# Optimization experiments

Hardware: AMD Instinct MI355X
Metric: run time of the kernel (lower is better)

Reference implementation:

```python
import jax, jax.numpy as jnp
import numpy as np

GROUP_SIZE = 64

def setup_inputs() -> dict:
    key = jax.random.key(0)
    ks = jax.random.split(key, 7)
    T, N, K, NG = 4096, 4096, 11264, 4096 // GROUP_SIZE
    x = jax.random.normal(ks[0], (T, N), dtype=jnp.float32)
    Q = jax.random.randint(ks[1], (K, N), 0, 8, dtype=jnp.int32)  # uint8 3-bit codes
    scales = jax.random.uniform(ks[2], (K, NG), dtype=jnp.float32)
    zeros = jax.random.uniform(ks[3], (K, NG), dtype=jnp.float32) * 7.0
    mu1 = jax.random.uniform(ks[4], (N,), dtype=jnp.float32) + 0.5
    mu2 = jax.random.uniform(ks[5], (K,), dtype=jnp.float32) + 0.5
    bias = jax.random.normal(ks[6], (K,), dtype=jnp.float32)
    return {"x": x, "Q": Q, "scales": scales, "zeros": zeros, "mu1": mu1, "mu2": mu2, "bias": bias}

def reference(x, Q, scales, zeros, mu1, mu2, bias):
    K, N = Q.shape
    ng = scales.shape[1]
    # group-wise dequant: (Q - zero) * scale, groups along N
    Qg = Q.astype(jnp.float32).reshape(K, ng, GROUP_SIZE)
    W_deq_norm = ((Qg - zeros[:, :, None]) * scales[:, :, None]).reshape(K, N)
    # Sinkhorn mu rescale: per-row mu2, per-column mu1
    W_deq = W_deq_norm * mu2[:, None] * mu1[None, :]
    out = x @ W_deq.T + bias
    return out
```

## Files before the change

kernel.cpp:

```cpp
#include <hip/hip_runtime.h>
#include <stdint.h>
#include <stddef.h>


typedef __attribute__((ext_vector_type(8))) short bfrag;
typedef __attribute__((ext_vector_type(4))) float f32x4;
typedef __attribute__((ext_vector_type(4))) int   i32x4;

__device__ __forceinline__ short f2bf(float f) {
    uint32_t u = __float_as_uint(f);
    u += 0x7fffu + ((u >> 16) & 1u);
    return (short)(u >> 16);
}

__device__ __forceinline__ void gload_lds16(const void* g, void* l) {
    __builtin_amdgcn_global_load_lds(
        (const __attribute__((address_space(1))) void*)g,
        (__attribute__((address_space(3))) void*)l,
        16, 0, 0);
}

__global__ void cvt_x_kernel(const float* __restrict__ x, short* __restrict__ xb) {
    int i = blockIdx.x * 256 + threadIdx.x;
    const f32x4* xv = (const f32x4*)x;
    f32x4 a = xv[2 * i];
    f32x4 b = xv[2 * i + 1];
    bfrag o;
    o[0] = f2bf(a[0]); o[1] = f2bf(a[1]); o[2] = f2bf(a[2]); o[3] = f2bf(a[3]);
    o[4] = f2bf(b[0]); o[5] = f2bf(b[1]); o[6] = f2bf(b[2]); o[7] = f2bf(b[3]);
    ((bfrag*)xb)[i] = o;
}

__global__ void deq_w_kernel(const int* __restrict__ Q,
                             const float* __restrict__ scales,
                             const float* __restrict__ zeros,
                             const float* __restrict__ mu1,
                             const float* __restrict__ mu2,
                             short* __restrict__ wb,
                             int k0, int N, int NG) {
    int kl = blockIdx.y;
    int kg = k0 + kl;
    int c  = blockIdx.x * 256 + threadIdx.x;
    int n0 = c << 3;
    int g  = n0 >> 6;
    float s = scales[(size_t)kg * NG + g] * mu2[kg];
    float z = zeros[(size_t)kg * NG + g];
    const i32x4* qv = (const i32x4*)(Q + (size_t)kg * N + n0);
    i32x4 q0 = qv[0];
    i32x4 q1 = qv[1];
    const f32x4* uv = (const f32x4*)(mu1 + n0);
    f32x4 u0 = uv[0];
    f32x4 u1 = uv[1];
    bfrag o;
    o[0] = f2bf(((float)q0[0] - z) * s * u0[0]);
    o[1] = f2bf(((float)q0[1] - z) * s * u0[1]);
    o[2] = f2bf(((float)q0[2] - z) * s * u0[2]);
    o[3] = f2bf(((float)q0[3] - z) * s * u0[3]);
    o[4] = f2bf(((float)q1[0] - z) * s * u1[0]);
    o[5] = f2bf(((float)q1[1] - z) * s * u1[1]);
    o[6] = f2bf(((float)q1[2] - z) * s * u1[2]);
    o[7] = f2bf(((float)q1[3] - z) * s * u1[3]);
    ((bfrag*)wb)[(size_t)kl * (N >> 3) + c] = o;
}

#define BM 128
#define BN 128
#define BK 32

__global__ void gemm_bt_kernel(const short* __restrict__ A,
                               const short* __restrict__ B,
                               const float* __restrict__ bias,
                               float* __restrict__ C,
                               int Kc, int Nout, int col0) {
    __shared__ __attribute__((aligned(16))) short As[BM * BK];
    __shared__ __attribute__((aligned(16))) short Bs[BN * BK];

    const int tid  = threadIdx.x;
    const int lane = tid & 63;
    const int wave = tid >> 6;
    const int wm   = (wave >> 1) * 64;
    const int wn   = (wave & 1) * 64;
    const int bm   = blockIdx.y * BM;
    const int bnl  = blockIdx.x * BN;

    f32x4 acc[4][4];
#pragma unroll
    for (int i = 0; i < 4; i++)
#pragma unroll
        for (int j = 0; j < 4; j++)
            acc[i][j] = (f32x4){0.f, 0.f, 0.f, 0.f};

    const short* gA  = A + (size_t)(bm + (tid >> 2)) * Kc + (tid & 3) * 8;
    const short* gA2 = gA + (size_t)64 * Kc;
    const short* gB  = B + (size_t)(bnl + (tid >> 2)) * Kc + (tid & 3) * 8;
    const short* gB2 = gB + (size_t)64 * Kc;
    short* lA  = As + tid * 8;
    short* lA2 = As + 2048 + tid * 8;
    short* lB  = Bs + tid * 8;
    short* lB2 = Bs + 2048 + tid * 8;

    const int r  = lane & 15;
    const int ko = (lane >> 4) * 8;
    const short* pa = As + (wm + r) * BK + ko;
    const short* pb = Bs + (wn + r) * BK + ko;

    for (int k0 = 0; k0 < Kc; k0 += BK) {
        gload_lds16(gA + k0, lA);
        gload_lds16(gA2 + k0, lA2);
        gload_lds16(gB + k0, lB);
        gload_lds16(gB2 + k0, lB2);
        __syncthreads();

        bfrag af[4], bfv[4];
#pragma unroll
        for (int i = 0; i < 4; i++) af[i]  = *(const bfrag*)(pa + i * 16 * BK);
#pragma unroll
        for (int j = 0; j < 4; j++) bfv[j] = *(const bfrag*)(pb + j * 16 * BK);

#pragma unroll
        for (int i = 0; i < 4; i++)
#pragma unroll
            for (int j = 0; j < 4; j++)
                acc[i][j] = __builtin_amdgcn_mfma_f32_16x16x32_bf16(
                    af[i], bfv[j], acc[i][j], 0, 0, 0);

        __syncthreads();
    }

    const int row0  = bm + wm + (lane >> 4) * 4;
    const int colg0 = col0 + bnl + wn;
#pragma unroll
    for (int j = 0; j < 4; j++) {
        int col  = colg0 + j * 16 + r;
        float bv = bias[col];
#pragma unroll
        for (int i = 0; i < 4; i++) {
            int row = row0 + i * 16;
#pragma unroll
            for (int q = 0; q < 4; q++)
                C[(size_t)(row + q) * Nout + col] = acc[i][j][q] + bv;
        }
    }
}

__global__ void naive_kernel(const float* __restrict__ x, const int* __restrict__ Q,
                             const float* __restrict__ scales, const float* __restrict__ zeros,
                             const float* __restrict__ mu1, const float* __restrict__ mu2,
                             const float* __restrict__ bias, float* __restrict__ out,
                             int T, int N, int K, int NG) {
    long long total = (long long)T * K;
    for (long long idx = blockIdx.x * 256ll + threadIdx.x; idx < total;
         idx += (long long)gridDim.x * 256ll) {
        int t = (int)(idx / K);
        int k = (int)(idx - (long long)t * K);
        float s = 0.f;
        for (int n = 0; n < N; n++) {
            int g = n >> 6;
            float w = ((float)Q[(size_t)k * N + n] - zeros[(size_t)k * NG + g]) *
                      scales[(size_t)k * NG + g];
            s += x[(size_t)t * N + n] * w * mu1[n];
        }
        out[idx] = s * mu2[k] + bias[k];
    }
}

extern "C" void kernel_launch(void* const* d_in, const int* in_sizes, int n_in,
                              void* d_out, int out_size, void* d_ws, size_t ws_size,
                              hipStream_t stream) {
    const float* x      = (const float*)d_in[0];
    const int*   Q      = (const int*)d_in[1];
    const float* scales = (const float*)d_in[2];
    const float* zeros  = (const float*)d_in[3];
    const float* mu1    = (const float*)d_in[4];
    const float* mu2    = (const float*)d_in[5];
    const float* bias   = (const float*)d_in[6];
    float* out = (float*)d_out;

    const int N  = in_sizes[4];
    const int K  = in_sizes[5];
    const int T  = in_sizes[0] / N;
    const int NG = in_sizes[2] / K;

    const size_t xb_bytes  = (size_t)T * N * 2;
    const size_t row_bytes = (size_t)N * 2;

    if (ws_size < xb_bytes + 128 * row_bytes) {
        naive_kernel<<<4096, 256, 0, stream>>>(x, Q, scales, zeros, mu1, mu2,
                                               bias, out, T, N, K, NG);
        return;
    }

    short* xb = (short*)d_ws;
    short* wb = (short*)((char*)d_ws + xb_bytes);
    size_t max_rows = (ws_size - xb_bytes) / row_bytes;
    int CH = (int)((max_rows / 128) * 128);
    if (CH > K) CH = K;

    cvt_x_kernel<<<(T * N / 8) / 256, 256, 0, stream>>>(x, xb);

    for (int c0 = 0; c0 < K; c0 += CH) {
        int rows = (K - c0 < CH) ? (K - c0) : CH;
        dim3 dgrid(N / (8 * 256), rows);
        deq_w_kernel<<<dgrid, 256, 0, stream>>>(Q, scales, zeros, mu1, mu2, wb,
                                                c0, N, NG);
        dim3 ggrid(rows / BN, T / BM);
        gemm_bt_kernel<<<ggrid, 256, 0, stream>>>(xb, wb, bias, out, N, K, c0);
    }
}
```

Measured before the change: 791.4 us.

## Replace GEMM with 256x256 tile, double-buffered, swizzled-LDS 8-phase pipelined kernel

Replaces the 128x128x32 single-buffered GEMM with a 512-thread 256x256x64 kernel. It double-buffers 128KB of LDS, uses an XOR-swizzled LDS layout to avoid bank conflicts, and interleaves global-to-LDS loads with MFMA phases using s_setprio and fine-grained waitcnt. It also remaps blocks for L2 locality and widens the convert and dequant kernels to 16 elements per thread. The aim is to raise arithmetic intensity and overlap memory with compute, at the cost of high register and LDS use and a stricter shape requirement.

```diff
diff --git a/kernel.cpp b/kernel.cpp
--- a/kernel.cpp
+++ b/kernel.cpp
@@ -21,14 +21,16 @@
 }
 
 __global__ void cvt_x_kernel(const float* __restrict__ x, short* __restrict__ xb) {
-    int i = blockIdx.x * 256 + threadIdx.x;
-    const f32x4* xv = (const f32x4*)x;
-    f32x4 a = xv[2 * i];
-    f32x4 b = xv[2 * i + 1];
-    bfrag o;
-    o[0] = f2bf(a[0]); o[1] = f2bf(a[1]); o[2] = f2bf(a[2]); o[3] = f2bf(a[3]);
-    o[4] = f2bf(b[0]); o[5] = f2bf(b[1]); o[6] = f2bf(b[2]); o[7] = f2bf(b[3]);
-    ((bfrag*)xb)[i] = o;
+    size_t i = (size_t)blockIdx.x * 256 + threadIdx.x;
+    const f32x4* xv = (const f32x4*)x + 4 * i;
+    f32x4 a = xv[0], b = xv[1], c = xv[2], d = xv[3];
+    bfrag o0, o1;
+    o0[0] = f2bf(a[0]); o0[1] = f2bf(a[1]); o0[2] = f2bf(a[2]); o0[3] = f2bf(a[3]);
+    o0[4] = f2bf(b[0]); o0[5] = f2bf(b[1]); o0[6] = f2bf(b[2]); o0[7] = f2bf(b[3]);
+    o1[0] = f2bf(c[0]); o1[1] = f2bf(c[1]); o1[2] = f2bf(c[2]); o1[3] = f2bf(c[3]);
+    o1[4] = f2bf(d[0]); o1[5] = f2bf(d[1]); o1[6] = f2bf(d[2]); o1[7] = f2bf(d[3]);
+    bfrag* ov = (bfrag*)xb + 2 * i;
+    ov[0] = o0; ov[1] = o1;
 }
 
 __global__ void deq_w_kernel(const int* __restrict__ Q,
@@ -38,106 +40,149 @@
                              const float* __restrict__ mu2,
                              short* __restrict__ wb,
                              int k0, int N, int NG) {
-    int kl = blockIdx.y;
-    int kg = k0 + kl;
-    int c  = blockIdx.x * 256 + threadIdx.x;
-    int n0 = c << 3;
-    int g  = n0 >> 6;
-    float s = scales[(size_t)kg * NG + g] * mu2[kg];
-    float z = zeros[(size_t)kg * NG + g];
+    const int kl = blockIdx.x;
+    const int kg = k0 + kl;
+    const int t  = threadIdx.x;
+    const int n0 = t << 4;
+    const int g  = n0 >> 6;
+    const float s = scales[(size_t)kg * NG + g] * mu2[kg];
+    const float z = zeros[(size_t)kg * NG + g];
     const i32x4* qv = (const i32x4*)(Q + (size_t)kg * N + n0);
-    i32x4 q0 = qv[0];
-    i32x4 q1 = qv[1];
     const f32x4* uv = (const f32x4*)(mu1 + n0);
-    f32x4 u0 = uv[0];
-    f32x4 u1 = uv[1];
-    bfrag o;
-    o[0] = f2bf(((float)q0[0] - z) * s * u0[0]);
-    o[1] = f2bf(((float)q0[1] - z) * s * u0[1]);
-    o[2] = f2bf(((float)q0[2] - z) * s * u0[2]);
-    o[3] = f2bf(((float)q0[3] - z) * s * u0[3]);
-    o[4] = f2bf(((float)q1[0] - z) * s * u1[0]);
-    o[5] = f2bf(((float)q1[1] - z) * s * u1[1]);
-    o[6] = f2bf(((float)q1[2] - z) * s * u1[2]);
-    o[7] = f2bf(((float)q1[3] - z) * s * u1[3]);
-    ((bfrag*)wb)[(size_t)kl * (N >> 3) + c] = o;
-}
-
-#define BM 128
-#define BN 128
-#define BK 32
-
-__global__ void gemm_bt_kernel(const short* __restrict__ A,
-                               const short* __restrict__ B,
-                               const float* __restrict__ bias,
-                               float* __restrict__ C,
-                               int Kc, int Nout, int col0) {
-    __shared__ __attribute__((aligned(16))) short As[BM * BK];
-    __shared__ __attribute__((aligned(16))) short Bs[BN * BK];
+    i32x4 q0 = qv[0], q1 = qv[1], q2 = qv[2], q3 = qv[3];
+    f32x4 u0 = uv[0], u1 = uv[1], u2 = uv[2], u3 = uv[3];
+    bfrag o0, o1;
+    o0[0] = f2bf(((float)q0[0] - z) * s * u0[0]);
+    o0[1] = f2bf(((float)q0[1] - z) * s * u0[1]);
+    o0[2] = f2bf(((float)q0[2] - z) * s * u0[2]);
+    o0[3] = f2bf(((float)q0[3] - z) * s * u0[3]);
+    o0[4] = f2bf(((float)q1[0] - z) * s * u1[0]);
+    o0[5] = f2bf(((float)q1[1] - z) * s * u1[1]);
+    o0[6] = f2bf(((float)q1[2] - z) * s * u1[2]);
+    o0[7] = f2bf(((float)q1[3] - z) * s * u1[3]);
+    o1[0] = f2bf(((float)q2[0] - z) * s * u2[0]);
+    o1[1] = f2bf(((float)q2[1] - z) * s * u2[1]);
+    o1[2] = f2bf(((float)q2[2] - z) * s * u2[2]);
+    o1[3] = f2bf(((float)q2[3] - z) * s * u2[3]);
+    o1[4] = f2bf(((float)q3[0] - z) * s * u3[0]);
+    o1[5] = f2bf(((float)q3[1] - z) * s * u3[1]);
+    o1[6] = f2bf(((float)q3[2] - z) * s * u3[2]);
+    o1[7] = f2bf(((float)q3[3] - z) * s * u3[3]);
+    bfrag* ov = (bfrag*)(wb + (size_t)kl * N + n0);
+    ov[0] = o0; ov[1] = o1;
+}
+
+
+__global__ __launch_bounds__(512, 2)
+void gemm8p_kernel(const short* __restrict__ A, const short* __restrict__ B,
+                   const float* __restrict__ bias, float* __restrict__ C,
+                   int Kc, int Nout, int col0, int GX) {
+    extern __shared__ __attribute__((aligned(16))) char smem[];
 
     const int tid  = threadIdx.x;
     const int lane = tid & 63;
-    const int wave = tid >> 6;
-    const int wm   = (wave >> 1) * 64;
-    const int wn   = (wave & 1) * 64;
-    const int bm   = blockIdx.y * BM;
-    const int bnl  = blockIdx.x * BN;
-
-    f32x4 acc[4][4];
-#pragma unroll
-    for (int i = 0; i < 4; i++)
+    const int wid  = tid >> 6;
+    const int wm   = wid >> 2;
+    const int wn   = wid & 3;
+    const int r    = lane & 15;
+    const int hib  = (lane >> 4) << 4;
+    const int sw   = (r & 7) << 4;
+
+    const int nwg = (int)gridDim.x;
+    const int cpx = nwg >> 3;
+    const int bid = (int)blockIdx.x;
+    const int swz = (bid & 7) * cpx + (bid >> 3);
+    const int bx  = swz % GX;
+    const int by  = swz / GX;
+    const int bm  = by * 256;
+    const int bnl = bx * 256;
+
+    const int KB = Kc * 2;
+    const int swcol = ((tid ^ (tid >> 3)) & 7) << 4;
+    const char* srcA = (const char*)A + (size_t)(bm  + (tid >> 3)) * KB + swcol;
+    const char* srcB = (const char*)B + (size_t)(bnl + (tid >> 3)) * KB + swcol;
+
+    f32x4 acc[8][4];
+#pragma unroll
+    for (int i = 0; i < 8; i++)
 #pragma unroll
         for (int j = 0; j < 4; j++)
             acc[i][j] = (f32x4){0.f, 0.f, 0.f, 0.f};
 
-    const short* gA  = A + (size_t)(bm + (tid >> 2)) * Kc + (tid & 3) * 8;
-    const short* gA2 = gA + (size_t)64 * Kc;
-    const short* gB  = B + (size_t)(bnl + (tid >> 2)) * Kc + (tid & 3) * 8;
-    const short* gB2 = gB + (size_t)64 * Kc;
-    short* lA  = As + tid * 8;
-    short* lA2 = As + 2048 + tid * 8;
-    short* lB  = Bs + tid * 8;
-    short* lB2 = Bs + 2048 + tid * 8;
-
-    const int r  = lane & 15;
-    const int ko = (lane >> 4) * 8;
-    const short* pa = As + (wm + r) * BK + ko;
-    const short* pb = Bs + (wn + r) * BK + ko;
-
-    for (int k0 = 0; k0 < Kc; k0 += BK) {
-        gload_lds16(gA + k0, lA);
-        gload_lds16(gA2 + k0, lA2);
-        gload_lds16(gB + k0, lB);
-        gload_lds16(gB2 + k0, lB2);
-        __syncthreads();
-
-        bfrag af[4], bfv[4];
-#pragma unroll
-        for (int i = 0; i < 4; i++) af[i]  = *(const bfrag*)(pa + i * 16 * BK);
-#pragma unroll
-        for (int j = 0; j < 4; j++) bfv[j] = *(const bfrag*)(pb + j * 16 * BK);
-
-#pragma unroll
-        for (int i = 0; i < 4; i++)
-#pragma unroll
-            for (int j = 0; j < 4; j++)
-                acc[i][j] = __builtin_amdgcn_mfma_f32_16x16x32_bf16(
-                    af[i], bfv[j], acc[i][j], 0, 0, 0);
-
-        __syncthreads();
-    }
-
-    const int row0  = bm + wm + (lane >> 4) * 4;
-    const int colg0 = col0 + bnl + wn;
-#pragma unroll
-    for (int j = 0; j < 4; j++) {
-        int col  = colg0 + j * 16 + r;
-        float bv = bias[col];
-#pragma unroll
-        for (int i = 0; i < 4; i++) {
-            int row = row0 + i * 16;
-#pragma unroll
-            for (int q = 0; q < 4; q++)
+    const int NT = Kc / 64;
+
+#define STG_A(t, q) gload_lds16(srcA + (size_t)(t) * 128 + (size_t)(q) * 64 * KB, \
+                                smem + ((t) & 1) * 65536 + (q) * 8192 + (tid << 4))
+#define STG_B(t, q) gload_lds16(srcB + (size_t)(t) * 128 + (size_t)(q) * 64 * KB, \
+                                smem + ((t) & 1) * 65536 + 32768 + (q) * 8192 + (tid << 4))
+#define LDF(base, row, s) (*(const bfrag*)((base) + (size_t)(row) * 128 + (((s) * 64 + hib) ^ sw)))
+#define MM(I, J, AF, BF) acc[I][J] = __builtin_amdgcn_mfma_f32_16x16x32_bf16(AF, BF, acc[I][J], 0, 0, 0)
+
+#define PH(BUF, MQ, NQ, STAGES, VM) do {                                        \
+    const char* Ab_ = smem + (BUF) * 65536;                                     \
+    const char* Bb_ = Ab_ + 32768;                                              \
+    const int ra_ = wm * 128 + (MQ) * 64 + r;                                   \
+    const int rb_ = wn * 64 + (NQ) * 32 + r;                                    \
+    bfrag a00_ = LDF(Ab_, ra_,      0), a01_ = LDF(Ab_, ra_,      1);           \
+    bfrag a10_ = LDF(Ab_, ra_ + 16, 0), a11_ = LDF(Ab_, ra_ + 16, 1);           \
+    bfrag a20_ = LDF(Ab_, ra_ + 32, 0), a21_ = LDF(Ab_, ra_ + 32, 1);           \
+    bfrag a30_ = LDF(Ab_, ra_ + 48, 0), a31_ = LDF(Ab_, ra_ + 48, 1);           \
+    bfrag b00_ = LDF(Bb_, rb_,      0), b01_ = LDF(Bb_, rb_,      1);           \
+    bfrag b10_ = LDF(Bb_, rb_ + 16, 0), b11_ = LDF(Bb_, rb_ + 16, 1);           \
+    STAGES;                                                                     \
+    __builtin_amdgcn_s_barrier();                                               \
+    asm volatile("s_waitcnt lgkmcnt(0)" ::: "memory");                          \
+    __builtin_amdgcn_s_setprio(1);                                              \
+    MM((MQ)*4 + 0, (NQ)*2 + 0, a00_, b00_); MM((MQ)*4 + 0, (NQ)*2 + 0, a01_, b01_); \
+    MM((MQ)*4 + 0, (NQ)*2 + 1, a00_, b10_); MM((MQ)*4 + 0, (NQ)*2 + 1, a01_, b11_); \
+    MM((MQ)*4 + 1, (NQ)*2 + 0, a10_, b00_); MM((MQ)*4 + 1, (NQ)*2 + 0, a11_, b01_); \
+    MM((MQ)*4 + 1, (NQ)*2 + 1, a10_, b10_); MM((MQ)*4 + 1, (NQ)*2 + 1, a11_, b11_); \
+    MM((MQ)*4 + 2, (NQ)*2 + 0, a20_, b00_); MM((MQ)*4 + 2, (NQ)*2 + 0, a21_, b01_); \
+    MM((MQ)*4 + 2, (NQ)*2 + 1, a20_, b10_); MM((MQ)*4 + 2, (NQ)*2 + 1, a21_, b11_); \
+    MM((MQ)*4 + 3, (NQ)*2 + 0, a30_, b00_); MM((MQ)*4 + 3, (NQ)*2 + 0, a31_, b01_); \
+    MM((MQ)*4 + 3, (NQ)*2 + 1, a30_, b10_); MM((MQ)*4 + 3, (NQ)*2 + 1, a31_, b11_); \
+    __builtin_amdgcn_s_setprio(0);                                              \
+    VM;                                                                         \
+    __builtin_amdgcn_s_barrier();                                               \
+} while (0)
+
+    STG_A(0, 0); STG_A(0, 1); STG_A(0, 2); STG_A(0, 3);
+    STG_B(0, 0); STG_B(0, 1); STG_B(0, 2); STG_B(0, 3);
+    STG_A(1, 0); STG_A(1, 2);
+    asm volatile("s_waitcnt vmcnt(2)" ::: "memory");
+    __builtin_amdgcn_s_barrier();
+
+    for (int it = 0; it < NT / 2; ++it) {
+        const int tb = 2 * it + 1;
+        int tc = 2 * it + 2; if (tc > NT - 1) tc = NT - 1;
+        int td = 2 * it + 3; if (td > NT - 1) td = NT - 1;
+        PH(0, 0, 0, { STG_A(tb, 1); STG_A(tb, 3); STG_B(tb, 0); }, (void)0);
+        PH(0, 0, 1, { STG_B(tb, 1); STG_B(tb, 2); STG_B(tb, 3); }, (void)0);
+        PH(0, 1, 0, { STG_A(tc, 0); STG_A(tc, 2); }, (void)0);
+        PH(0, 1, 1, {}, asm volatile("s_waitcnt vmcnt(2)" ::: "memory"));
+        PH(1, 0, 0, { STG_A(tc, 1); STG_A(tc, 3); STG_B(tc, 0); }, (void)0);
+        PH(1, 0, 1, { STG_B(tc, 1); STG_B(tc, 2); STG_B(tc, 3); }, (void)0);
+        PH(1, 1, 0, { STG_A(td, 0); STG_A(td, 2); }, (void)0);
+        PH(1, 1, 1, {}, asm volatile("s_waitcnt vmcnt(2)" ::: "memory"));
+    }
+
+#undef PH
+#undef MM
+#undef LDF
+#undef STG_A
+#undef STG_B
+
+    const int row0 = bm + wm * 128 + (lane >> 4) * 4;
+    const int colg = col0 + bnl + wn * 64 + r;
+#pragma unroll
+    for (int j = 0; j < 4; ++j) {
+        const int col = colg + j * 16;
+        const float bv = bias[col];
+#pragma unroll
+        for (int i = 0; i < 8; ++i) {
+            const int row = row0 + i * 16;
+#pragma unroll
+            for (int q = 0; q < 4; ++q)
                 C[(size_t)(row + q) * Nout + col] = acc[i][j][q] + bv;
         }
     }
@@ -184,26 +229,38 @@
     const size_t xb_bytes  = (size_t)T * N * 2;
     const size_t row_bytes = (size_t)N * 2;
 
-    if (ws_size < xb_bytes + 128 * row_bytes) {
+    const bool shape_ok = (T % 256 == 0) && (K % 256 == 0) &&
+                          (N % 128 == 0) && (N % 64 == 0);
+
+    if (!shape_ok || ws_size < xb_bytes + 256 * row_bytes) {
         naive_kernel<<<4096, 256, 0, stream>>>(x, Q, scales, zeros, mu1, mu2,
                                                bias, out, T, N, K, NG);
         return;
     }
 
+    static bool attr_done = false;
+    if (!attr_done) {
+        (void)hipFuncSetAttribute(reinterpret_cast<const void*>(gemm8p_kernel),
+                                  hipFuncAttributeMaxDynamicSharedMemorySize,
+                                  131072);
+        attr_done = true;
+    }
+
     short* xb = (short*)d_ws;
     short* wb = (short*)((char*)d_ws + xb_bytes);
     size_t max_rows = (ws_size - xb_bytes) / row_bytes;
-    int CH = (int)((max_rows / 128) * 128);
+    int CH = (int)((max_rows / 256) * 256);
     if (CH > K) CH = K;
 
-    cvt_x_kernel<<<(T * N / 8) / 256, 256, 0, stream>>>(x, xb);
+    cvt_x_kernel<<<(T * N / 16) / 256, 256, 0, stream>>>(x, xb);
 
     for (int c0 = 0; c0 < K; c0 += CH) {
         int rows = (K - c0 < CH) ? (K - c0) : CH;
-        dim3 dgrid(N / (8 * 256), rows);
-        deq_w_kernel<<<dgrid, 256, 0, stream>>>(Q, scales, zeros, mu1, mu2, wb,
-                                                c0, N, NG);
-        dim3 ggrid(rows / BN, T / BM);
-        gemm_bt_kernel<<<ggrid, 256, 0, stream>>>(xb, wb, bias, out, N, K, c0);
-    }
-}
+        deq_w_kernel<<<rows, 256, 0, stream>>>(Q, scales, zeros, mu1, mu2, wb,
+                                               c0, N, NG);
+        const int GX = rows / 256;
+        dim3 ggrid(GX * (T / 256));
+        gemm8p_kernel<<<ggrid, 512, 131072, stream>>>(xb, wb, bias, out,
+                                                      N, K, c0, GX);
+    }
+}
```

New measurement: 732.5 us. -7.5%, faster.
